# Performance work log

Hardware: AMD Instinct MI355X
Metric: run time of the kernel (lower is better)

## Reference

```python
import jax, jax.numpy as jnp
import numpy as np

N = 86016      # 1024 graphs x 84 nodes
E = 4194304    # directed edges
H = 32         # hidden size
B = 1024       # graphs per batch
NPG = 84       # nodes per graph (hardcoded in original forward)
DEPTH = 4      # args.depth
NEG_SLOPE = 0.2


def setup_inputs() -> dict:
    key = jax.random.key(0)
    ks = jax.random.split(key, 12)
    s = 0.1
    return {
        "x": jax.random.normal(ks[0], (N, 1), jnp.float32),
        "edge_index": jax.random.randint(ks[1], (2, E), 0, N, jnp.int64 if jax.config.jax_enable_x64 else jnp.int32),
        "edge_attr": jax.random.normal(ks[2], (E, 2), jnp.float32),
        "W0": jax.random.normal(ks[3], (1, H), jnp.float32) * s,
        "Ws": jax.random.normal(ks[4], (DEPTH - 1, H, H), jnp.float32) * s,
        "att_src": jax.random.normal(ks[5], (DEPTH, H), jnp.float32) * s,
        "att_dst": jax.random.normal(ks[6], (DEPTH, H), jnp.float32) * s,
        "We": jax.random.normal(ks[7], (DEPTH, 2, H), jnp.float32) * s,
        "att_edge": jax.random.normal(ks[8], (DEPTH, H), jnp.float32) * s,
        "bias": jnp.zeros((DEPTH, H), jnp.float32),
        "lin_w": jax.random.normal(ks[9], (H, 1), jnp.float32) * s,
        "lin_b": jnp.zeros((1,), jnp.float32),
    }


def _gat_layer(h_in, src, dst, ea, W, a_s, a_d, We_l, a_e, b):
    """PyG GATConv, heads=1, edge_dim set, self-loops already appended.
    src/dst: [E+N] indices; ea: [E+N, edge_dim] edge attrs (with mean-filled loops)."""
    h = h_in @ W                                  # [N, H]
    alpha_src = h @ a_s                           # [N]
    alpha_dst = h @ a_d                           # [N]
    # fold lin_edge + att_edge: (ea @ We) @ a_e == ea @ (We @ a_e) -> avoids [E,H]
    alpha_edge = ea @ (We_l @ a_e)                # [E+N]
    logits = alpha_src[src] + alpha_dst[dst] + alpha_edge
    logits = jnp.where(logits >= 0, logits, NEG_SLOPE * logits)  # leaky_relu(0.2)
    # segment softmax over destination nodes (every node has a self-loop -> nonempty)
    m = jax.ops.segment_max(logits, dst, num_segments=N)
    w = jnp.exp(logits - m[dst])
    denom = jax.ops.segment_sum(w, dst, num_segments=N)
    alpha = w / denom[dst]                        # [E+N]
    out = jax.ops.segment_sum(alpha[:, None] * h[src], dst, num_segments=N)
    return out + b


def reference(x, edge_index, edge_attr, W0, Ws, att_src, att_dst, We, att_edge, bias, lin_w, lin_b):
    src0, dst0 = edge_index[0], edge_index[1]
    # add_self_loops with fill_value='mean': per-dst mean of incoming edge attrs
    deg = jax.ops.segment_sum(jnp.ones((E,), x.dtype), dst0, num_segments=N)
    ea_loop = jax.ops.segment_sum(edge_attr, dst0, num_segments=N) / jnp.maximum(deg, 1.0)[:, None]
    loops = jnp.arange(N, dtype=src0.dtype)
    src = jnp.concatenate([src0, loops])
    dst = jnp.concatenate([dst0, loops])
    ea = jnp.concatenate([edge_attr, ea_loop], axis=0)

    # layer 0 (+ relu; dropout is identity in eval)
    h = _gat_layer(x, src, dst, ea, W0, att_src[0], att_dst[0], We[0], att_edge[0], bias[0])
    h = jax.nn.relu(h)
    # middle layers
    for i in range(1, DEPTH - 1):
        h = _gat_layer(h, src, dst, ea, Ws[i - 1], att_src[i], att_dst[i], We[i], att_edge[i], bias[i])
        h = jax.nn.relu(h)
    # last layer: no relu/dropout
    h = _gat_layer(h, src, dst, ea, Ws[DEPTH - 2], att_src[DEPTH - 1], att_dst[DEPTH - 1],
                   We[DEPTH - 1], att_edge[DEPTH - 1], bias[DEPTH - 1])

    # global_add_pool over 84-node graphs, then linear + relu
    graph_ids = jnp.repeat(jnp.arange(B), NPG)    # [N]
    pooled = jax.ops.segment_sum(h, graph_ids, num_segments=B)  # [B, H]
    return jax.nn.relu(pooled @ lin_w + lin_b)    # [B, 1]
```

## Files before the change

kernel.cpp:

```cpp
#include <hip/hip_runtime.h>

#define N_NODES 86016
#define N_EDGES 4194304
#define HID 32
#define B_GR 1024
#define NPG 84
#define NEG 0.2f

#define NCH 512
#define CHE 8192
#define NB  512
#define NPB 168
#define SRCMASK 0x1FFFF

typedef float floatx2 __attribute__((ext_vector_type(2)));
typedef float f32x4 __attribute__((ext_vector_type(4)));
typedef short bf16x8 __attribute__((ext_vector_type(8)));

constexpr size_t O_REC   = 0;
constexpr size_t O_CM    = O_REC  + (size_t)N_EDGES * 8;
constexpr size_t O_HT    = O_CM   + (size_t)NB * NCH * 4;
constexpr size_t O_HB    = O_HT   + (size_t)N_NODES * HID;
constexpr size_t O_AS    = O_HB   + (size_t)N_NODES * HID * 4;
constexpr size_t O_AD    = O_AS   + (size_t)N_NODES * 4;
constexpr size_t O_ROW   = O_AD   + (size_t)N_NODES * 4;
constexpr size_t O_BTOT  = O_ROW  + (size_t)(N_NODES + 1) * 4 + 12;
constexpr size_t O_BBASE = O_BTOT + (size_t)NB * 4;
constexpr size_t O_FOLD  = O_BBASE + (size_t)(NB + 1) * 4 + 12;

__device__ __forceinline__ unsigned short f2bf(float f) {
    unsigned u = __float_as_uint(f);
    u += 0x7FFFu + ((u >> 16) & 1u);
    return (unsigned short)(u >> 16);
}

__global__ __launch_bounds__(1024) void k_hist(const int* __restrict__ dst, int* __restrict__ cm) {
    __shared__ int cnt[NB];
    int t = threadIdx.x, c = blockIdx.x;
    if (t < NB) cnt[t] = 0;
    __syncthreads();
    int base = c * CHE;
#pragma unroll
    for (int k = 0; k < 8; ++k) {
        int d = dst[base + k * 1024 + t];
        atomicAdd(&cnt[(unsigned)d / NPB], 1);
    }
    __syncthreads();
    if (t < NB) cm[t * NCH + c] = cnt[t];
}

__global__ __launch_bounds__(512) void k_scanchunks(int* __restrict__ cm, int* __restrict__ btot) {
    __shared__ int sa[NCH], sb[NCH];
    int b = blockIdx.x, t = threadIdx.x;
    sa[t] = cm[b * NCH + t];
    __syncthreads();
    int* s = sa; int* d = sb;
    for (int off = 1; off < NCH; off <<= 1) {
        d[t] = s[t] + (t >= off ? s[t - off] : 0);
        __syncthreads();
        int* tmp = s; s = d; d = tmp;
    }
    cm[b * NCH + t] = t ? s[t - 1] : 0;
    if (t == 0) btot[b] = s[NCH - 1];
}

__global__ void k_scanbuckets(const int* __restrict__ btot, int* __restrict__ bbase,
                              int* __restrict__ row,
                              const float* __restrict__ We, const float* __restrict__ ae,
                              float* __restrict__ fold) {
    __shared__ int sa[NB], sb[NB];
    int t = threadIdx.x;
    if (t < 8) {
        int l = t >> 1, c = t & 1;
        float s = 0.f;
        for (int j = 0; j < 32; ++j) s += We[l * 64 + c * 32 + j] * ae[l * 32 + j];
        fold[t] = s;
    }
    sa[t] = btot[t];
    __syncthreads();
    int* s = sa; int* d = sb;
    for (int off = 1; off < NB; off <<= 1) {
        d[t] = s[t] + (t >= off ? s[t - off] : 0);
        __syncthreads();
        int* tmp = s; s = d; d = tmp;
    }
    bbase[t] = t ? s[t - 1] : 0;
    if (t == NB - 1) { bbase[NB] = s[NB - 1]; row[N_NODES] = s[NB - 1]; }
}

__global__ __launch_bounds__(1024) void k_place(const int* __restrict__ ei,
                                                const float2* __restrict__ ea,
                                                const int* __restrict__ cm,
                                                const int* __restrict__ bbase,
                                                int2* __restrict__ rec) {
    __shared__ int cnt[NB];
    __shared__ int base[NB];
    int t = threadIdx.x, c = blockIdx.x;
    if (t < NB) cnt[t] = 0;
    __syncthreads();
    int eb = c * CHE;
    int wd0[8], bin[8], rnk[8];
    unsigned pk[8];
#pragma unroll
    for (int k = 0; k < 8; ++k) {
        int e = eb + k * 1024 + t;
        int s = ei[e];
        int d = ei[N_EDGES + e];
        float2 a = ea[e];
        int b = (unsigned)d / NPB;
        int dn = d - b * NPB;
        wd0[k] = s | (dn << 17);
        pk[k] = ((unsigned)f2bf(a.y) << 16) | f2bf(a.x);
        bin[k] = b;
        rnk[k] = atomicAdd(&cnt[b], 1);
    }
    __syncthreads();
    if (t < NB) base[t] = bbase[t] + cm[t * NCH + c];
    __syncthreads();
#pragma unroll
    for (int k = 0; k < 8; ++k)
        rec[base[bin[k]] + rnk[k]] = make_int2(wd0[k], (int)pk[k]);
}

__global__ __launch_bounds__(1024) void k_sort(int2* __restrict__ rec,
                                               const int* __restrict__ bbase,
                                               int* __restrict__ row) {
    __shared__ int cnt[256], tmp[256], ebase[256];
    int b = blockIdx.x, t = threadIdx.x;
    int n0 = b * NPB;
    int beg = bbase[b], end = bbase[b + 1], m = end - beg;
    if (t < 256) cnt[t] = 0;
    __syncthreads();
    int2 rv[12];
    int dr[12];
    int cv = 0;
    for (int i = t; i < m; i += 1024) {
        int2 r = rec[beg + i];
        int dn = ((unsigned)r.x >> 17) & 0xFF;
        int rnk = atomicAdd(&cnt[dn], 1);
        if (cv < 12) { rv[cv] = r; dr[cv] = dn | (rnk << 8); }
        cv++;
    }
    __syncthreads();
    int* s = cnt; int* d = tmp;
    for (int off = 1; off < 256; off <<= 1) {
        int v = 0;
        if (t < 256) v = s[t] + (t >= off ? s[t - off] : 0);
        __syncthreads();
        if (t < 256) d[t] = v;
        __syncthreads();
        int* tp = s; s = d; d = tp;
    }
    if (t < 256) ebase[t] = t ? s[t - 1] : 0;
    __syncthreads();
    if (t < NPB) row[n0 + t] = beg + ebase[t];
    int ncv = cv < 12 ? cv : 12;
    for (int k = 0; k < ncv; ++k) {
        int dn = dr[k] & 0xFF;
        int rnk = dr[k] >> 8;
        rec[beg + ebase[dn] + rnk] = rv[k];
    }
}

__device__ __forceinline__ void store_fp8_pair(unsigned short* __restrict__ hout,
                                               int n, int j, float acc) {
    float p = __shfl_xor(acc, 1);
    if (!(j & 1)) {
        int pk = __builtin_amdgcn_cvt_pk_fp8_f32(acc, p, 0, false);
        hout[(n << 4) + (j >> 1)] = (unsigned short)pk;
    }
}

__global__ void k_transform0(const float* __restrict__ x, const float* __restrict__ W0,
                             const float* __restrict__ as_w, const float* __restrict__ ad_w,
                             unsigned short* __restrict__ hout, float* __restrict__ as_arr,
                             float* __restrict__ ad_arr) {
    int tid = blockIdx.x * 256 + threadIdx.x;
    int j = tid & 31;
    int n = tid >> 5;
    float acc = x[n] * W0[j];
    store_fp8_pair(hout, n, j, acc);
    float v1 = acc * as_w[j], v2 = acc * ad_w[j];
#pragma unroll
    for (int m = 16; m >= 1; m >>= 1) {
        v1 += __shfl_xor(v1, m);
        v2 += __shfl_xor(v2, m);
    }
    if (j == 0) { as_arr[n] = v1; ad_arr[n] = v2; }
}

__global__ void k_transform_m(const float* __restrict__ hin, const float* __restrict__ W,
                              const float* __restrict__ as_w, const float* __restrict__ ad_w,
                              unsigned short* __restrict__ hout, float* __restrict__ as_arr,
                              float* __restrict__ ad_arr) {
    int lane = threadIdx.x & 63;
    int wv = threadIdx.x >> 6;
    int col = lane & 15, hi = lane >> 4;
    int nb = (blockIdx.x * 4 + wv) * 64;
    bf16x8 b0, b1;
#pragma unroll
    for (int e = 0; e < 8; ++e) {
        b0[e] = (short)f2bf(W[(hi * 8 + e) * 32 + col]);
        b1[e] = (short)f2bf(W[(hi * 8 + e) * 32 + col + 16]);
    }
    float asw0 = as_w[col], asw1 = as_w[col + 16];
    float adw0 = ad_w[col], adw1 = ad_w[col + 16];
    float4 a0[4], a1[4];
#pragma unroll
    for (int t = 0; t < 4; ++t) {
        const float* r = hin + (size_t)(nb + t * 16 + col) * 32 + hi * 8;
        a0[t] = *(const float4*)r;
        a1[t] = *(const float4*)(r + 4);
    }
    int* hw = (int*)hout;
#pragma unroll
    for (int t = 0; t < 4; ++t) {
        bf16x8 a;
        a[0] = (short)f2bf(a0[t].x); a[1] = (short)f2bf(a0[t].y);
        a[2] = (short)f2bf(a0[t].z); a[3] = (short)f2bf(a0[t].w);
        a[4] = (short)f2bf(a1[t].x); a[5] = (short)f2bf(a1[t].y);
        a[6] = (short)f2bf(a1[t].z); a[7] = (short)f2bf(a1[t].w);
        f32x4 z = {0.f, 0.f, 0.f, 0.f};
        f32x4 c0 = __builtin_amdgcn_mfma_f32_16x16x32_bf16(a, b0, z, 0, 0, 0);
        f32x4 c1 = __builtin_amdgcn_mfma_f32_16x16x32_bf16(a, b1, z, 0, 0, 0);
        int n0t = nb + t * 16;
#pragma unroll
        for (int i = 0; i < 4; ++i) {
            float pa = c0[i] * asw0 + c1[i] * asw1;
            float pd = c0[i] * adw0 + c1[i] * adw1;
#pragma unroll
            for (int m = 1; m <= 8; m <<= 1) {
                pa += __shfl_xor(pa, m);
                pd += __shfl_xor(pd, m);
            }
            float e0 = __shfl_xor(c0[i], 1), e1 = __shfl_xor(c1[i], 1);
            int pk0 = __builtin_amdgcn_cvt_pk_fp8_f32(c0[i], e0, 0, false);
            int pk1 = __builtin_amdgcn_cvt_pk_fp8_f32(c1[i], e1, 0, false);
            int q0 = __shfl_xor(pk0, 2), q1 = __shfl_xor(pk1, 2);
            int n = n0t + hi * 4 + i;
            if ((col & 3) == 0) {
                int w0 = (pk0 & 0xFFFF) | (q0 << 16);
                int w1 = (pk1 & 0xFFFF) | (q1 << 16);
                hw[(n << 3) + (col >> 2)] = w0;
                hw[(n << 3) + 4 + (col >> 2)] = w1;
            }
            if (col == 0) { as_arr[n] = pa; ad_arr[n] = pd; }
        }
    }
}

__device__ __forceinline__ void acc_word(float wp, int word, floatx2* acc) {
    floatx2 v01 = __builtin_amdgcn_cvt_pk_f32_fp8(word, false);
    floatx2 v23 = __builtin_amdgcn_cvt_pk_f32_fp8(word, true);
    floatx2 w2 = {wp, wp};
    acc[0] = __builtin_elementwise_fma(w2, v01, acc[0]);
    acc[1] = __builtin_elementwise_fma(w2, v23, acc[1]);
}

__global__ void k_gather(const unsigned short* __restrict__ hT, const int2* __restrict__ rec,
                         const int* __restrict__ row,
                         const float* __restrict__ as_arr, const float* __restrict__ ad_arr,
                         const float* __restrict__ fold, const float* __restrict__ bias,
                         float* __restrict__ out, int do_relu) {
    const int* hw = (const int*)hT;
    __shared__ int2   exS[4][64];
    __shared__ float2 exW[4][64];
    int lane = threadIdx.x & 63;
    int wv = threadIdx.x >> 6;
    int slot = lane >> 3;
    int dl = lane & 7;
    const int* hwd = hw + dl;
    int nb = blockIdx.x * 16 + wv * 4;
    int rowv[5];
#pragma unroll
    for (int i = 0; i < 5; ++i) rowv[i] = row[nb + i];
    float f0 = fold[0], f1 = fold[1];
    float4 bi = *(const float4*)(bias + 4 * dl);
    floatx2 zz = {0.f, 0.f};

    int2 r0[2], r1[2];
#pragma unroll
    for (int k = 0; k < 2; ++k) {
        int beg0 = rowv[2 * k], end0 = rowv[2 * k + 1];
        int beg1 = rowv[2 * k + 1], end1 = rowv[2 * k + 2];
        int i0 = beg0 + lane; i0 = (i0 < end0) ? i0 : 0;
        int i1 = beg1 + lane; i1 = (i1 < end1) ? i1 : 0;
        r0[k] = rec[i0];
        r1[k] = rec[i1];
    }

#pragma unroll
    for (int k = 0; k < 2; ++k) {
        int beg0 = rowv[2 * k], end0 = rowv[2 * k + 1];
        int beg1 = rowv[2 * k + 1], end1 = rowv[2 * k + 2];
        int n0 = nb + 2 * k, n1 = n0 + 1;
        bool act0 = (beg0 + lane) < end0;
        bool act1 = (beg1 + lane) < end1;
        int s0 = r0[k].x & SRCMASK;
        int s1 = r1[k].x & SRCMASK;
        exS[wv][lane] = make_int2(s0 << 3, s1 << 3);
        int h0[8], h1[8];
#pragma unroll
        for (int p = 0; p < 8; ++p) {
            int2 sp = exS[wv][p * 8 + slot];
            h0[p] = hwd[sp.x];
            h1[p] = hwd[sp.y];
        }
        float a0 = as_arr[s0], a1 = as_arr[s1];
        float cd0 = ad_arr[n0], cd1 = ad_arr[n1];
        float ax0 = __uint_as_float((unsigned)r0[k].y << 16);
        float ay0 = __uint_as_float((unsigned)r0[k].y & 0xFFFF0000u);
        float ax1 = __uint_as_float((unsigned)r1[k].y << 16);
        float ay1 = __uint_as_float((unsigned)r1[k].y & 0xFFFF0000u);
        float ed0 = fmaf(ax0, f0, ay0 * f1);
        float ed1 = fmaf(ax1, f0, ay1 * f1);
        float lg0 = a0 + cd0 + ed0; lg0 = fmaxf(lg0, NEG * lg0);
        float lg1 = a1 + cd1 + ed1; lg1 = fmaxf(lg1, NEG * lg1);
        float w0 = act0 ? __expf(lg0) : 0.f;
        float w1 = act1 ? __expf(lg1) : 0.f;
        exW[wv][lane] = make_float2(w0, w1);
        float den0 = w0, den1 = w1;
        float es0 = act0 ? ed0 : 0.f;
        float es1 = act1 ? ed1 : 0.f;
        floatx2 acc0[2] = {zz, zz};
        floatx2 acc1[2] = {zz, zz};
#pragma unroll
        for (int p = 0; p < 8; ++p) {
            float2 wp = exW[wv][p * 8 + slot];
            acc_word(wp.x, h0[p], acc0);
            acc_word(wp.y, h1[p], acc1);
        }
        if (end0 - beg0 > 64 || end1 - beg1 > 64) {
            for (int e0 = beg0 + 64, e1 = beg1 + 64; e0 < end0 || e1 < end1;
                 e0 += 64, e1 += 64) {
                int i0 = e0 + lane; bool c0 = i0 < end0; i0 = c0 ? i0 : 0;
                int i1 = e1 + lane; bool c1 = i1 < end1; i1 = c1 ? i1 : 0;
                int2 q0 = rec[i0], q1 = rec[i1];
                int t0 = q0.x & SRCMASK, t1 = q1.x & SRCMASK;
                exS[wv][lane] = make_int2(t0 << 3, t1 << 3);
                int g0[8], g1[8];
#pragma unroll
                for (int p = 0; p < 8; ++p) {
                    int2 sp = exS[wv][p * 8 + slot];
                    g0[p] = hwd[sp.x];
                    g1[p] = hwd[sp.y];
                }
                float b0 = as_arr[t0], b1 = as_arr[t1];
                float bx0 = __uint_as_float((unsigned)q0.y << 16);
                float by0 = __uint_as_float((unsigned)q0.y & 0xFFFF0000u);
                float bx1 = __uint_as_float((unsigned)q1.y << 16);
                float by1 = __uint_as_float((unsigned)q1.y & 0xFFFF0000u);
                float fd0 = fmaf(bx0, f0, by0 * f1);
                float fd1 = fmaf(bx1, f0, by1 * f1);
                float mg0 = b0 + cd0 + fd0; mg0 = fmaxf(mg0, NEG * mg0);
                float mg1 = b1 + cd1 + fd1; mg1 = fmaxf(mg1, NEG * mg1);
                float v0 = c0 ? __expf(mg0) : 0.f;
                float v1 = c1 ? __expf(mg1) : 0.f;
                exW[wv][lane] = make_float2(v0, v1);
                den0 += v0; den1 += v1;
                es0 += c0 ? fd0 : 0.f;
                es1 += c1 ? fd1 : 0.f;
#pragma unroll
                for (int p = 0; p < 8; ++p) {
                    float2 wp = exW[wv][p * 8 + slot];
                    acc_word(wp.x, g0[p], acc0);
                    acc_word(wp.y, g1[p], acc1);
                }
            }
        }
        float* fA = (float*)acc0;
        float* fB = (float*)acc1;
#pragma unroll
        for (int m = 8; m <= 32; m <<= 1) {
#pragma unroll
            for (int q = 0; q < 4; ++q) {
                fA[q] += __shfl_xor(fA[q], m);
                fB[q] += __shfl_xor(fB[q], m);
            }
        }
#pragma unroll
        for (int m = 1; m <= 32; m <<= 1) {
            den0 += __shfl_xor(den0, m);
            den1 += __shfl_xor(den1, m);
            es0 += __shfl_xor(es0, m);
            es1 += __shfl_xor(es1, m);
        }
        int dg0 = end0 - beg0, dg1 = end1 - beg1;
        float el0 = es0 / fmaxf((float)dg0, 1.0f);
        float el1 = es1 / fmaxf((float)dg1, 1.0f);
        float lgs0 = as_arr[n0] + cd0 + el0; lgs0 = fmaxf(lgs0, NEG * lgs0);
        float lgs1 = as_arr[n1] + cd1 + el1; lgs1 = fmaxf(lgs1, NEG * lgs1);
        float ws0 = __expf(lgs0), ws1 = __expf(lgs1);
        den0 += ws0; den1 += ws1;
        acc_word(ws0, hwd[n0 << 3], acc0);
        acc_word(ws1, hwd[n1 << 3], acc1);
        float rd0 = 1.0f / den0, rd1 = 1.0f / den1;
        float4 o0 = {fA[0] * rd0 + bi.x, fA[1] * rd0 + bi.y,
                     fA[2] * rd0 + bi.z, fA[3] * rd0 + bi.w};
        float4 o1 = {fB[0] * rd1 + bi.x, fB[1] * rd1 + bi.y,
                     fB[2] * rd1 + bi.z, fB[3] * rd1 + bi.w};
        if (do_relu) {
            o0.x = fmaxf(o0.x, 0.f); o0.y = fmaxf(o0.y, 0.f);
            o0.z = fmaxf(o0.z, 0.f); o0.w = fmaxf(o0.w, 0.f);
            o1.x = fmaxf(o1.x, 0.f); o1.y = fmaxf(o1.y, 0.f);
            o1.z = fmaxf(o1.z, 0.f); o1.w = fmaxf(o1.w, 0.f);
        }
        if (slot == 0) {
            *(float4*)(out + (n0 << 5) + (dl << 2)) = o0;
            *(float4*)(out + (n1 << 5) + (dl << 2)) = o1;
        }
    }
}

__global__ void k_pool(const float* __restrict__ h, const float* __restrict__ lw,
                       const float* __restrict__ lb, float* __restrict__ out) {
    int lane = threadIdx.x & 63;
    int g = blockIdx.x * 4 + (threadIdx.x >> 6);
    int j = lane & 31;
    int half = lane >> 5;
    const float* base = h + (size_t)g * NPG * HID;
    float acc = 0.f;
    for (int i = half; i < NPG; i += 2) acc += base[i * HID + j];
    acc += __shfl_xor(acc, 32);
    float v = acc * lw[j];
#pragma unroll
    for (int m = 16; m >= 1; m >>= 1) v += __shfl_xor(v, m);
    if (lane == 0) out[g] = fmaxf(v + lb[0], 0.f);
}

extern "C" void kernel_launch(void* const* d_in, const int* in_sizes, int n_in,
                              void* d_out, int out_size, void* d_ws, size_t ws_size,
                              hipStream_t stream) {
    const float* x        = (const float*)d_in[0];
    const int*   ei       = (const int*)d_in[1];
    const float* eattr    = (const float*)d_in[2];
    const float* W0       = (const float*)d_in[3];
    const float* Ws       = (const float*)d_in[4];
    const float* att_src  = (const float*)d_in[5];
    const float* att_dst  = (const float*)d_in[6];
    const float* We       = (const float*)d_in[7];
    const float* att_edge = (const float*)d_in[8];
    const float* bias     = (const float*)d_in[9];
    const float* lin_w    = (const float*)d_in[10];
    const float* lin_b    = (const float*)d_in[11];
    float* out = (float*)d_out;

    char* w = (char*)d_ws;
    int2*           rec    = (int2*)(w + O_REC);
    int*            cm     = (int*)(w + O_CM);
    unsigned short* hT     = (unsigned short*)(w + O_HT);
    float*          hB     = (float*)(w + O_HB);
    float*          as_arr = (float*)(w + O_AS);
    float*          ad_arr = (float*)(w + O_AD);
    int*            row    = (int*)(w + O_ROW);
    int*            btot   = (int*)(w + O_BTOT);
    int*            bbase  = (int*)(w + O_BBASE);
    float*          fold   = (float*)(w + O_FOLD);

    k_hist<<<NCH, 1024, 0, stream>>>(ei + N_EDGES, cm);
    k_scanchunks<<<NB, 512, 0, stream>>>(cm, btot);
    k_scanbuckets<<<1, NB, 0, stream>>>(btot, bbase, row, We, att_edge, fold);
    k_place<<<NCH, 1024, 0, stream>>>(ei, (const float2*)eattr, cm, bbase, rec);
    k_sort<<<NB, 1024, 0, stream>>>(rec, bbase, row);

    k_transform0<<<N_NODES * HID / 256, 256, 0, stream>>>(x, W0, att_src, att_dst,
                                                          hT, as_arr, ad_arr);
    k_gather<<<N_NODES / 16, 256, 0, stream>>>(hT, rec, row, as_arr, ad_arr,
                                               fold, bias, hB, 1);
    for (int l = 1; l < 4; ++l) {
        k_transform_m<<<N_NODES / 256, 256, 0, stream>>>(
            hB, Ws + (size_t)(l - 1) * HID * HID, att_src + l * HID, att_dst + l * HID,
            hT, as_arr, ad_arr);
        k_gather<<<N_NODES / 16, 256, 0, stream>>>(hT, rec, row, as_arr, ad_arr,
                                                   fold + 2 * l, bias + l * HID, hB,
                                                   (l < 3) ? 1 : 0);
    }

    k_pool<<<B_GR / 4, 256, 0, stream>>>(hB, lin_w, lin_b, out);
}
```

Measured before the change: 433.4 us.

## Replace two-pass bucket sort with per-node counting sort via global atomics

After: 799.1 us. +84.4%, slower.

```diff
diff --git a/kernel.cpp b/kernel.cpp
--- a/kernel.cpp
+++ b/kernel.cpp
@@ -7,10 +7,6 @@
 #define NPG 84
 #define NEG 0.2f
 
-#define NCH 512
-#define CHE 8192
-#define NB  512
-#define NPB 168
 #define SRCMASK 0x1FFFF
 
 typedef float floatx2 __attribute__((ext_vector_type(2)));
@@ -18,15 +14,16 @@
 typedef short bf16x8 __attribute__((ext_vector_type(8)));
 
 constexpr size_t O_REC   = 0;
-constexpr size_t O_CM    = O_REC  + (size_t)N_EDGES * 8;
-constexpr size_t O_HT    = O_CM   + (size_t)NB * NCH * 4;
+constexpr size_t O_CNT   = O_REC  + (size_t)N_EDGES * 8;
+constexpr size_t O_PTR   = O_CNT  + (size_t)N_NODES * 4;
+constexpr size_t O_HT    = O_PTR  + (size_t)N_NODES * 4;
 constexpr size_t O_HB    = O_HT   + (size_t)N_NODES * HID;
 constexpr size_t O_AS    = O_HB   + (size_t)N_NODES * HID * 4;
 constexpr size_t O_AD    = O_AS   + (size_t)N_NODES * 4;
 constexpr size_t O_ROW   = O_AD   + (size_t)N_NODES * 4;
 constexpr size_t O_BTOT  = O_ROW  + (size_t)(N_NODES + 1) * 4 + 12;
-constexpr size_t O_BBASE = O_BTOT + (size_t)NB * 4;
-constexpr size_t O_FOLD  = O_BBASE + (size_t)(NB + 1) * 4 + 12;
+constexpr size_t O_BBASE = O_BTOT + (size_t)128 * 4;
+constexpr size_t O_FOLD  = O_BBASE + (size_t)128 * 4;
 
 __device__ __forceinline__ unsigned short f2bf(float f) {
     unsigned u = __float_as_uint(f);
@@ -34,41 +31,42 @@
     return (unsigned short)(u >> 16);
 }
 
-__global__ __launch_bounds__(1024) void k_hist(const int* __restrict__ dst, int* __restrict__ cm) {
-    __shared__ int cnt[NB];
-    int t = threadIdx.x, c = blockIdx.x;
-    if (t < NB) cnt[t] = 0;
-    __syncthreads();
-    int base = c * CHE;
-#pragma unroll
-    for (int k = 0; k < 8; ++k) {
-        int d = dst[base + k * 1024 + t];
-        atomicAdd(&cnt[(unsigned)d / NPB], 1);
-    }
-    __syncthreads();
-    if (t < NB) cm[t * NCH + c] = cnt[t];
-}
-
-__global__ __launch_bounds__(512) void k_scanchunks(int* __restrict__ cm, int* __restrict__ btot) {
-    __shared__ int sa[NCH], sb[NCH];
+
+__global__ __launch_bounds__(1024) void k_zero(int* __restrict__ cnt) {
+    cnt[blockIdx.x * 1024 + threadIdx.x] = 0;
+}
+
+__global__ __launch_bounds__(1024) void k_histn(const int* __restrict__ dst,
+                                                int* __restrict__ cnt) {
+    int e0 = blockIdx.x * 8192 + threadIdx.x;
+    int d[8];
+#pragma unroll
+    for (int k = 0; k < 8; ++k) d[k] = dst[e0 + k * 1024];
+#pragma unroll
+    for (int k = 0; k < 8; ++k) atomicAdd(&cnt[d[k]], 1);
+}
+
+__global__ __launch_bounds__(1024) void k_scanA(int* __restrict__ cnt,
+                                                int* __restrict__ btot) {
+    __shared__ int sa[1024], sb[1024];
     int b = blockIdx.x, t = threadIdx.x;
-    sa[t] = cm[b * NCH + t];
+    int v = cnt[b * 1024 + t];
+    sa[t] = v;
     __syncthreads();
     int* s = sa; int* d = sb;
-    for (int off = 1; off < NCH; off <<= 1) {
+    for (int off = 1; off < 1024; off <<= 1) {
         d[t] = s[t] + (t >= off ? s[t - off] : 0);
         __syncthreads();
         int* tmp = s; s = d; d = tmp;
     }
-    cm[b * NCH + t] = t ? s[t - 1] : 0;
-    if (t == 0) btot[b] = s[NCH - 1];
-}
-
-__global__ void k_scanbuckets(const int* __restrict__ btot, int* __restrict__ bbase,
-                              int* __restrict__ row,
-                              const float* __restrict__ We, const float* __restrict__ ae,
-                              float* __restrict__ fold) {
-    __shared__ int sa[NB], sb[NB];
+    cnt[b * 1024 + t] = s[t] - v;
+    if (t == 1023) btot[b] = s[1023];
+}
+
+__global__ void k_scanB(const int* __restrict__ btot, int* __restrict__ bbase,
+                        const float* __restrict__ We, const float* __restrict__ ae,
+                        float* __restrict__ fold) {
+    __shared__ int sa[128], sb[128];
     int t = threadIdx.x;
     if (t < 8) {
         int l = t >> 1, c = t & 1;
@@ -76,90 +74,50 @@
         for (int j = 0; j < 32; ++j) s += We[l * 64 + c * 32 + j] * ae[l * 32 + j];
         fold[t] = s;
     }
-    sa[t] = btot[t];
+    int v = (t < 84) ? btot[t] : 0;
+    sa[t] = v;
     __syncthreads();
     int* s = sa; int* d = sb;
-    for (int off = 1; off < NB; off <<= 1) {
+    for (int off = 1; off < 128; off <<= 1) {
         d[t] = s[t] + (t >= off ? s[t - off] : 0);
         __syncthreads();
         int* tmp = s; s = d; d = tmp;
     }
-    bbase[t] = t ? s[t - 1] : 0;
-    if (t == NB - 1) { bbase[NB] = s[NB - 1]; row[N_NODES] = s[NB - 1]; }
-}
-
-__global__ __launch_bounds__(1024) void k_place(const int* __restrict__ ei,
-                                                const float2* __restrict__ ea,
-                                                const int* __restrict__ cm,
+    if (t < 84) bbase[t] = s[t] - v;
+}
+
+__global__ __launch_bounds__(1024) void k_scanC(const int* __restrict__ cnt,
                                                 const int* __restrict__ bbase,
-                                                int2* __restrict__ rec) {
-    __shared__ int cnt[NB];
-    __shared__ int base[NB];
-    int t = threadIdx.x, c = blockIdx.x;
-    if (t < NB) cnt[t] = 0;
-    __syncthreads();
-    int eb = c * CHE;
-    int wd0[8], bin[8], rnk[8];
+                                                int* __restrict__ row,
+                                                int* __restrict__ ptr) {
+    int b = blockIdx.x, t = threadIdx.x;
+    int n = b * 1024 + t;
+    int v = cnt[n] + bbase[b];
+    row[n] = v;
+    ptr[n] = v;
+    if (n == 0) row[N_NODES] = N_EDGES;
+}
+
+__global__ __launch_bounds__(1024) void k_placed(const int* __restrict__ ei,
+                                                 const float2* __restrict__ ea,
+                                                 int* __restrict__ ptr,
+                                                 int2* __restrict__ rec) {
+    int e0 = blockIdx.x * 8192 + threadIdx.x;
+    int s[8], d[8];
     unsigned pk[8];
 #pragma unroll
     for (int k = 0; k < 8; ++k) {
-        int e = eb + k * 1024 + t;
-        int s = ei[e];
-        int d = ei[N_EDGES + e];
+        int e = e0 + k * 1024;
+        s[k] = ei[e];
+        d[k] = ei[N_EDGES + e];
         float2 a = ea[e];
-        int b = (unsigned)d / NPB;
-        int dn = d - b * NPB;
-        wd0[k] = s | (dn << 17);
         pk[k] = ((unsigned)f2bf(a.y) << 16) | f2bf(a.x);
-        bin[k] = b;
-        rnk[k] = atomicAdd(&cnt[b], 1);
-    }
-    __syncthreads();
-    if (t < NB) base[t] = bbase[t] + cm[t * NCH + c];
-    __syncthreads();
-#pragma unroll
-    for (int k = 0; k < 8; ++k)
-        rec[base[bin[k]] + rnk[k]] = make_int2(wd0[k], (int)pk[k]);
-}
-
-__global__ __launch_bounds__(1024) void k_sort(int2* __restrict__ rec,
-                                               const int* __restrict__ bbase,
-                                               int* __restrict__ row) {
-    __shared__ int cnt[256], tmp[256], ebase[256];
-    int b = blockIdx.x, t = threadIdx.x;
-    int n0 = b * NPB;
-    int beg = bbase[b], end = bbase[b + 1], m = end - beg;
-    if (t < 256) cnt[t] = 0;
-    __syncthreads();
-    int2 rv[12];
-    int dr[12];
-    int cv = 0;
-    for (int i = t; i < m; i += 1024) {
-        int2 r = rec[beg + i];
-        int dn = ((unsigned)r.x >> 17) & 0xFF;
-        int rnk = atomicAdd(&cnt[dn], 1);
-        if (cv < 12) { rv[cv] = r; dr[cv] = dn | (rnk << 8); }
-        cv++;
-    }
-    __syncthreads();
-    int* s = cnt; int* d = tmp;
-    for (int off = 1; off < 256; off <<= 1) {
-        int v = 0;
-        if (t < 256) v = s[t] + (t >= off ? s[t - off] : 0);
-        __syncthreads();
-        if (t < 256) d[t] = v;
-        __syncthreads();
-        int* tp = s; s = d; d = tp;
-    }
-    if (t < 256) ebase[t] = t ? s[t - 1] : 0;
-    __syncthreads();
-    if (t < NPB) row[n0 + t] = beg + ebase[t];
-    int ncv = cv < 12 ? cv : 12;
-    for (int k = 0; k < ncv; ++k) {
-        int dn = dr[k] & 0xFF;
-        int rnk = dr[k] >> 8;
-        rec[beg + ebase[dn] + rnk] = rv[k];
-    }
+    }
+    int pos[8];
+#pragma unroll
+    for (int k = 0; k < 8; ++k) pos[k] = atomicAdd(&ptr[d[k]], 1);
+#pragma unroll
+    for (int k = 0; k < 8; ++k) rec[pos[k]] = make_int2(s[k], (int)pk[k]);
 }
 
 __device__ __forceinline__ void store_fp8_pair(unsigned short* __restrict__ hout,
@@ -447,7 +405,8 @@
 
     char* w = (char*)d_ws;
     int2*           rec    = (int2*)(w + O_REC);
-    int*            cm     = (int*)(w + O_CM);
+    int*            cnt    = (int*)(w + O_CNT);
+    int*            ptr    = (int*)(w + O_PTR);
     unsigned short* hT     = (unsigned short*)(w + O_HT);
     float*          hB     = (float*)(w + O_HB);
     float*          as_arr = (float*)(w + O_AS);
@@ -457,11 +416,12 @@
     int*            bbase  = (int*)(w + O_BBASE);
     float*          fold   = (float*)(w + O_FOLD);
 
-    k_hist<<<NCH, 1024, 0, stream>>>(ei + N_EDGES, cm);
-    k_scanchunks<<<NB, 512, 0, stream>>>(cm, btot);
-    k_scanbuckets<<<1, NB, 0, stream>>>(btot, bbase, row, We, att_edge, fold);
-    k_place<<<NCH, 1024, 0, stream>>>(ei, (const float2*)eattr, cm, bbase, rec);
-    k_sort<<<NB, 1024, 0, stream>>>(rec, bbase, row);
+    k_zero<<<N_NODES / 1024, 1024, 0, stream>>>(cnt);
+    k_histn<<<N_EDGES / 8192, 1024, 0, stream>>>(ei + N_EDGES, cnt);
+    k_scanA<<<N_NODES / 1024, 1024, 0, stream>>>(cnt, btot);
+    k_scanB<<<1, 128, 0, stream>>>(btot, bbase, We, att_edge, fold);
+    k_scanC<<<N_NODES / 1024, 1024, 0, stream>>>(cnt, bbase, row, ptr);
+    k_placed<<<N_EDGES / 8192, 1024, 0, stream>>>(ei, (const float2*)eattr, ptr, rec);
 
     k_transform0<<<N_NODES * HID / 256, 256, 0, stream>>>(x, W0, att_src, att_dst,
                                                           hT, as_arr, ad_arr);
```

## Replace histogram-and-scan bucketing with fixed-capacity buckets and atomic cursors

Applied to the files above, without the earlier changes.

After: 436.7 us. No clear change (+0.8%).

```diff
diff --git a/kernel.cpp b/kernel.cpp
--- a/kernel.cpp
+++ b/kernel.cpp
@@ -11,6 +11,7 @@
 #define CHE 8192
 #define NB  512
 #define NPB 168
+#define CAP 12288
 #define SRCMASK 0x1FFFF
 
 typedef float floatx2 __attribute__((ext_vector_type(2)));
@@ -18,15 +19,13 @@
 typedef short bf16x8 __attribute__((ext_vector_type(8)));
 
 constexpr size_t O_REC   = 0;
-constexpr size_t O_CM    = O_REC  + (size_t)N_EDGES * 8;
-constexpr size_t O_HT    = O_CM   + (size_t)NB * NCH * 4;
+constexpr size_t O_CUR   = O_REC  + (size_t)NB * CAP * 8;
+constexpr size_t O_HT    = O_CUR  + (size_t)NB * 4 + 60;
 constexpr size_t O_HB    = O_HT   + (size_t)N_NODES * HID;
 constexpr size_t O_AS    = O_HB   + (size_t)N_NODES * HID * 4;
 constexpr size_t O_AD    = O_AS   + (size_t)N_NODES * 4;
-constexpr size_t O_ROW   = O_AD   + (size_t)N_NODES * 4;
-constexpr size_t O_BTOT  = O_ROW  + (size_t)(N_NODES + 1) * 4 + 12;
-constexpr size_t O_BBASE = O_BTOT + (size_t)NB * 4;
-constexpr size_t O_FOLD  = O_BBASE + (size_t)(NB + 1) * 4 + 12;
+constexpr size_t O_ROW2  = O_AD   + (size_t)N_NODES * 4;
+constexpr size_t O_FOLD  = O_ROW2 + (size_t)N_NODES * 8;
 
 __device__ __forceinline__ unsigned short f2bf(float f) {
     unsigned u = __float_as_uint(f);
@@ -34,41 +33,10 @@
     return (unsigned short)(u >> 16);
 }
 
-__global__ __launch_bounds__(1024) void k_hist(const int* __restrict__ dst, int* __restrict__ cm) {
-    __shared__ int cnt[NB];
-    int t = threadIdx.x, c = blockIdx.x;
-    if (t < NB) cnt[t] = 0;
-    __syncthreads();
-    int base = c * CHE;
-#pragma unroll
-    for (int k = 0; k < 8; ++k) {
-        int d = dst[base + k * 1024 + t];
-        atomicAdd(&cnt[(unsigned)d / NPB], 1);
-    }
-    __syncthreads();
-    if (t < NB) cm[t * NCH + c] = cnt[t];
-}
-
-__global__ __launch_bounds__(512) void k_scanchunks(int* __restrict__ cm, int* __restrict__ btot) {
-    __shared__ int sa[NCH], sb[NCH];
-    int b = blockIdx.x, t = threadIdx.x;
-    sa[t] = cm[b * NCH + t];
-    __syncthreads();
-    int* s = sa; int* d = sb;
-    for (int off = 1; off < NCH; off <<= 1) {
-        d[t] = s[t] + (t >= off ? s[t - off] : 0);
-        __syncthreads();
-        int* tmp = s; s = d; d = tmp;
-    }
-    cm[b * NCH + t] = t ? s[t - 1] : 0;
-    if (t == 0) btot[b] = s[NCH - 1];
-}
-
-__global__ void k_scanbuckets(const int* __restrict__ btot, int* __restrict__ bbase,
-                              int* __restrict__ row,
-                              const float* __restrict__ We, const float* __restrict__ ae,
-                              float* __restrict__ fold) {
-    __shared__ int sa[NB], sb[NB];
+
+__global__ void k_fold(int* __restrict__ cursor,
+                       const float* __restrict__ We, const float* __restrict__ ae,
+                       float* __restrict__ fold) {
     int t = threadIdx.x;
     if (t < 8) {
         int l = t >> 1, c = t & 1;
@@ -76,23 +44,13 @@
         for (int j = 0; j < 32; ++j) s += We[l * 64 + c * 32 + j] * ae[l * 32 + j];
         fold[t] = s;
     }
-    sa[t] = btot[t];
-    __syncthreads();
-    int* s = sa; int* d = sb;
-    for (int off = 1; off < NB; off <<= 1) {
-        d[t] = s[t] + (t >= off ? s[t - off] : 0);
-        __syncthreads();
-        int* tmp = s; s = d; d = tmp;
-    }
-    bbase[t] = t ? s[t - 1] : 0;
-    if (t == NB - 1) { bbase[NB] = s[NB - 1]; row[N_NODES] = s[NB - 1]; }
-}
-
-__global__ __launch_bounds__(1024) void k_place(const int* __restrict__ ei,
-                                                const float2* __restrict__ ea,
-                                                const int* __restrict__ cm,
-                                                const int* __restrict__ bbase,
-                                                int2* __restrict__ rec) {
+    cursor[t] = t * CAP;
+}
+
+__global__ __launch_bounds__(1024) void k_place2(const int* __restrict__ ei,
+                                                 const float2* __restrict__ ea,
+                                                 int* __restrict__ cursor,
+                                                 int2* __restrict__ rec) {
     __shared__ int cnt[NB];
     __shared__ int base[NB];
     int t = threadIdx.x, c = blockIdx.x;
@@ -115,20 +73,21 @@
         rnk[k] = atomicAdd(&cnt[b], 1);
     }
     __syncthreads();
-    if (t < NB) base[t] = bbase[t] + cm[t * NCH + c];
+    if (t < NB) base[t] = atomicAdd(&cursor[t], cnt[t]);
     __syncthreads();
 #pragma unroll
     for (int k = 0; k < 8; ++k)
         rec[base[bin[k]] + rnk[k]] = make_int2(wd0[k], (int)pk[k]);
 }
 
-__global__ __launch_bounds__(1024) void k_sort(int2* __restrict__ rec,
-                                               const int* __restrict__ bbase,
-                                               int* __restrict__ row) {
+__global__ __launch_bounds__(1024) void k_sort2(int2* __restrict__ rec,
+                                                const int* __restrict__ cursor,
+                                                int2* __restrict__ row2) {
     __shared__ int cnt[256], tmp[256], ebase[256];
     int b = blockIdx.x, t = threadIdx.x;
     int n0 = b * NPB;
-    int beg = bbase[b], end = bbase[b + 1], m = end - beg;
+    int beg = b * CAP;
+    int m = cursor[b] - beg;
     if (t < 256) cnt[t] = 0;
     __syncthreads();
     int2 rv[12];
@@ -153,7 +112,7 @@
     }
     if (t < 256) ebase[t] = t ? s[t - 1] : 0;
     __syncthreads();
-    if (t < NPB) row[n0 + t] = beg + ebase[t];
+    if (t < NPB) row2[n0 + t] = make_int2(beg + ebase[t], beg + ebase[t + 1]);
     int ncv = cv < 12 ? cv : 12;
     for (int k = 0; k < ncv; ++k) {
         int dn = dr[k] & 0xFF;
@@ -258,7 +217,7 @@
 }
 
 __global__ void k_gather(const unsigned short* __restrict__ hT, const int2* __restrict__ rec,
-                         const int* __restrict__ row,
+                         const int2* __restrict__ row2,
                          const float* __restrict__ as_arr, const float* __restrict__ ad_arr,
                          const float* __restrict__ fold, const float* __restrict__ bias,
                          float* __restrict__ out, int do_relu) {
@@ -271,9 +230,9 @@
     int dl = lane & 7;
     const int* hwd = hw + dl;
     int nb = blockIdx.x * 16 + wv * 4;
-    int rowv[5];
-#pragma unroll
-    for (int i = 0; i < 5; ++i) rowv[i] = row[nb + i];
+    int2 rv2[4];
+#pragma unroll
+    for (int i = 0; i < 4; ++i) rv2[i] = row2[nb + i];
     float f0 = fold[0], f1 = fold[1];
     float4 bi = *(const float4*)(bias + 4 * dl);
     floatx2 zz = {0.f, 0.f};
@@ -281,8 +240,8 @@
     int2 r0[2], r1[2];
 #pragma unroll
     for (int k = 0; k < 2; ++k) {
-        int beg0 = rowv[2 * k], end0 = rowv[2 * k + 1];
-        int beg1 = rowv[2 * k + 1], end1 = rowv[2 * k + 2];
+        int beg0 = rv2[2 * k].x, end0 = rv2[2 * k].y;
+        int beg1 = rv2[2 * k + 1].x, end1 = rv2[2 * k + 1].y;
         int i0 = beg0 + lane; i0 = (i0 < end0) ? i0 : 0;
         int i1 = beg1 + lane; i1 = (i1 < end1) ? i1 : 0;
         r0[k] = rec[i0];
@@ -291,8 +250,8 @@
 
 #pragma unroll
     for (int k = 0; k < 2; ++k) {
-        int beg0 = rowv[2 * k], end0 = rowv[2 * k + 1];
-        int beg1 = rowv[2 * k + 1], end1 = rowv[2 * k + 2];
+        int beg0 = rv2[2 * k].x, end0 = rv2[2 * k].y;
+        int beg1 = rv2[2 * k + 1].x, end1 = rv2[2 * k + 1].y;
         int n0 = nb + 2 * k, n1 = n0 + 1;
         bool act0 = (beg0 + lane) < end0;
         bool act1 = (beg1 + lane) < end1;
@@ -447,31 +406,27 @@
 
     char* w = (char*)d_ws;
     int2*           rec    = (int2*)(w + O_REC);
-    int*            cm     = (int*)(w + O_CM);
+    int*            cursor = (int*)(w + O_CUR);
     unsigned short* hT     = (unsigned short*)(w + O_HT);
     float*          hB     = (float*)(w + O_HB);
     float*          as_arr = (float*)(w + O_AS);
     float*          ad_arr = (float*)(w + O_AD);
-    int*            row    = (int*)(w + O_ROW);
-    int*            btot   = (int*)(w + O_BTOT);
-    int*            bbase  = (int*)(w + O_BBASE);
+    int2*           row2   = (int2*)(w + O_ROW2);
     float*          fold   = (float*)(w + O_FOLD);
 
-    k_hist<<<NCH, 1024, 0, stream>>>(ei + N_EDGES, cm);
-    k_scanchunks<<<NB, 512, 0, stream>>>(cm, btot);
-    k_scanbuckets<<<1, NB, 0, stream>>>(btot, bbase, row, We, att_edge, fold);
-    k_place<<<NCH, 1024, 0, stream>>>(ei, (const float2*)eattr, cm, bbase, rec);
-    k_sort<<<NB, 1024, 0, stream>>>(rec, bbase, row);
+    k_fold<<<1, NB, 0, stream>>>(cursor, We, att_edge, fold);
+    k_place2<<<NCH, 1024, 0, stream>>>(ei, (const float2*)eattr, cursor, rec);
+    k_sort2<<<NB, 1024, 0, stream>>>(rec, cursor, row2);
 
     k_transform0<<<N_NODES * HID / 256, 256, 0, stream>>>(x, W0, att_src, att_dst,
                                                           hT, as_arr, ad_arr);
-    k_gather<<<N_NODES / 16, 256, 0, stream>>>(hT, rec, row, as_arr, ad_arr,
+    k_gather<<<N_NODES / 16, 256, 0, stream>>>(hT, rec, row2, as_arr, ad_arr,
                                                fold, bias, hB, 1);
     for (int l = 1; l < 4; ++l) {
         k_transform_m<<<N_NODES / 256, 256, 0, stream>>>(
             hB, Ws + (size_t)(l - 1) * HID * HID, att_src + l * HID, att_dst + l * HID,
             hT, as_arr, ad_arr);
-        k_gather<<<N_NODES / 16, 256, 0, stream>>>(hT, rec, row, as_arr, ad_arr,
+        k_gather<<<N_NODES / 16, 256, 0, stream>>>(hT, rec, row2, as_arr, ad_arr,
                                                    fold + 2 * l, bias + l * HID, hB,
                                                    (l < 3) ? 1 : 0);
     }
```
